# Optimization experiments

Measured on AMD Instinct MI355X. Metric: run time of the kernel, lower is better.

The kernel has to match this reference:

```python
import jax, jax.numpy as jnp
import numpy as np

B, T, F_IN = 4, 2048, 768
G, V = 2, 320          # num_groups, num_vars per group
VQ_DIM = 256
D = VQ_DIM // G        # var_dim = 128


def setup_inputs() -> dict:
    key = jax.random.key(0)
    k1, k2, k3 = jax.random.split(key, 3)
    x = jax.random.normal(k1, (B, T, F_IN), dtype=jnp.float32)
    # weight_proj: Linear(input_dim -> G*V), weight init N(0,1), bias zeros
    W = jax.random.normal(k2, (G * V, F_IN), dtype=jnp.float32)
    b = jnp.zeros((G * V,), dtype=jnp.float32)
    # self.vars: uniform_(0,1), stored here reshaped as [G, V, D]
    codebook = jax.random.uniform(k3, (G, V, D), dtype=jnp.float32)
    return {"x": x, "W": W, "b": b, "codebook": codebook}


def reference(x, W, b, codebook):
    bsz, tsz, fsz = x.shape
    g, v, d = codebook.shape
    # projection to logits over (group, codeword)
    logits = (x.reshape(-1, fsz) @ W.T + b).reshape(-1, g, v)  # [BT, G, V]
    k = jnp.argmax(logits, axis=-1)                            # [BT, G] int
    # hard one-hot stats (code perplexity)
    hard = jax.nn.one_hot(k, v, dtype=jnp.float32)             # [BT, G, V]
    hard_probs = hard.mean(axis=0)                             # [G, V]
    code_perplexity = jnp.exp(-jnp.sum(hard_probs * jnp.log(hard_probs + 1e-7), axis=-1)).sum()
    # soft stats (prob perplexity)
    avg_probs = jax.nn.softmax(logits.astype(jnp.float32), axis=-1).mean(axis=0)  # [G, V]
    prob_perplexity = jnp.exp(-jnp.sum(avg_probs * jnp.log(avg_probs + 1e-7), axis=-1)).sum()
    # eval path: hard one-hot times codebook summed == direct gather of codewords
    xq = codebook[jnp.arange(g)[None, :], k]                   # [BT, G, D]
    xq = xq.reshape(bsz, tsz, g * d)                           # [B, T, vq_dim]
    return xq, g * v, code_perplexity, prob_perplexity
```

## Files before the change

kernel.cpp:

```cpp
#include <hip/hip_runtime.h>
#include <hip/hip_bf16.h>

#define NROWS 8192
#define KDIM  768
#define VSZ   320
#define GSZ   2
#define NCOL  640
#define DSZ   128
#define BM    64
#define NMT   (NROWS / BM)
#define NBLK  (NMT * 2)
#define XQ_TOTAL (NROWS * GSZ * DSZ)
#define MARGIN 0.75f
#define NSHARD 8

typedef __attribute__((ext_vector_type(8))) short bf16x8;
typedef __attribute__((ext_vector_type(4))) float f32x4;

static __device__ __forceinline__ short f2bf(float f) {
    union { __hip_bfloat16 h; short s; } u;
    u.h = __float2bfloat16(f);
    return u.s;
}

static __device__ __forceinline__ void gload_lds16(const void* g, void* l) {
    __builtin_amdgcn_global_load_lds(
        (const __attribute__((address_space(1))) void*)g,
        (__attribute__((address_space(3))) void*)l, 16, 0, 0);
}

__global__ __launch_bounds__(256) void prep_w_k(const float* __restrict__ W,
                                                short* __restrict__ Wb,
                                                float* __restrict__ accf) {
    if (blockIdx.x < 20) {
        const int i = blockIdx.x * 256 + threadIdx.x;
        accf[i] = 0.f;
        accf[i + 5120] = 0.f;
    }
    const int id   = blockIdx.x * 256 + threadIdx.x;
    const int lane = id & 63;
    const int f    = id >> 6;
    const int n    = f % 5;
    const int t2   = f / 5;
    const int hc   = t2 & 7;
    const int kb   = t2 >> 3;
    const int col  = (hc * 5 + n) * 16 + (lane & 15);
    const int k    = kb * 32 + (lane >> 4) * 8;
    const float4 a = *(const float4*)(W + (size_t)col * KDIM + k);
    const float4 c = *(const float4*)(W + (size_t)col * KDIM + k + 4);
    bf16x8 r;
    r[0] = f2bf(a.x); r[1] = f2bf(a.y); r[2] = f2bf(a.z); r[3] = f2bf(a.w);
    r[4] = f2bf(c.x); r[5] = f2bf(c.y); r[6] = f2bf(c.z); r[7] = f2bf(c.w);
    *(bf16x8*)(Wb + (size_t)id * 8) = r;
}

#define STAGEB(kb64, BUF) do {                                                 \
    _Pragma("unroll")                                                          \
    for (int j = 0; j < 3; ++j) {                                              \
        const int rm = (j == 0) ? w : (j == 1) ? (w + 16) : (32 + (w & 7));    \
        const int kf = rm / 20, rr = rm % 20;                                  \
        const short* srcp = Wb + ((size_t)((2 * (kb64) + kf) * 8 + hc0 + rr / 5) * 5 + rr % 5) * 512; \
        gload_lds16(srcp + lane * 8, (char*)(BUF) + 8192 + rm * 1024);         \
    }                                                                          \
} while (0)

#define AWRITE(BUF, v) do {                                                    \
    const short s0 = f2bf((v).x), s1 = f2bf((v).y);                            \
    const short s2 = f2bf((v).z), s3 = f2bf((v).w);                            \
    const int lo = (s0 & 0xffff) | ((int)s1 << 16);                            \
    const int hi = (s2 & 0xffff) | ((int)s3 << 16);                            \
    *(int2*)((char*)(BUF) + a_off) = make_int2(lo, hi);                        \
} while (0)

#define COMPUTE(BUF) do {                                                      \
    const char* _bp = (const char*)(BUF);                                      \
    const bf16x8 a0 = *(const bf16x8*)(_bp + (rs * 2 + 0) * 1024 + lane * 16); \
    const bf16x8 a1 = *(const bf16x8*)(_bp + (rs * 2 + 1) * 1024 + lane * 16); \
    bf16x8 b0_[5], b1_[5];                                                     \
    _Pragma("unroll")                                                          \
    for (int n = 0; n < 5; ++n) {                                              \
        b0_[n] = *(const bf16x8*)(_bp + 8192 + (cc * 5 + n) * 1024 + lane * 16);      \
        b1_[n] = *(const bf16x8*)(_bp + 8192 + (20 + cc * 5 + n) * 1024 + lane * 16); \
    }                                                                          \
    _Pragma("unroll")                                                          \
    for (int n = 0; n < 5; ++n)                                                \
        acc[n] = __builtin_amdgcn_mfma_f32_16x16x32_bf16(a0, b0_[n], acc[n], 0, 0, 0); \
    _Pragma("unroll")                                                          \
    for (int n = 0; n < 5; ++n)                                                \
        acc[n] = __builtin_amdgcn_mfma_f32_16x16x32_bf16(a1, b1_[n], acc[n], 0, 0, 0); \
} while (0)

#define SYNC(N) do {                                                           \
    asm volatile("s_waitcnt vmcnt(" #N ") lgkmcnt(0)" ::: "memory");           \
    __builtin_amdgcn_sched_barrier(0);                                         \
    __builtin_amdgcn_s_barrier();                                              \
} while (0)

#define PH(kk, BA, BS, BC) do {                                                \
    AWRITE(BA, xv1);                                                           \
    xv1 = xv2;                                                                 \
    STAGEB((kk) + 2, BS);                                                      \
    xv2 = *(const float4*)(xrow + ((kk) + 3) * 64);                            \
    COMPUTE(BC);                                                               \
    SYNC(4);                                                                   \
} while (0)

__global__ __launch_bounds__(1024, 4) void fused_vq_k(
    const short* __restrict__ Wb,
    const float* __restrict__ x, const float* __restrict__ W,
    const float* __restrict__ b, const float* __restrict__ codebook,
    float* __restrict__ accf, float* __restrict__ xq) {

    __shared__ __align__(16) char bufs[3][48 * 1024];
    __shared__ float pacc[4][VSZ];
    __shared__ float cnt_f[VSZ];
    __shared__ float wmax[BM][4];
    __shared__ int   warg[BM][4];
    __shared__ float ssum[BM][4];
    __shared__ float rmax_s[BM];
    __shared__ int   rarg_s[BM];
    __shared__ int   cnt_s[BM];
    __shared__ int   list_s[BM][16];
    __shared__ int   code_s[BM];
    __shared__ int   work_s[BM];
    __shared__ int   nwork_s;

    const int tid   = threadIdx.x;
    const int lane  = tid & 63;
    const int w     = tid >> 6;
    const int l15   = lane & 15;
    const int l4    = lane >> 4;
    const int xcd   = (int)blockIdx.x & 7;
    const int sb    = xcd * (NBLK / 8) + ((int)blockIdx.x >> 3);
    const int mt    = sb >> 1;
    const int h     = sb & 1;
    const int row0  = mt * BM;
    const int rs    = w >> 2;
    const int cc    = w & 3;
    const int rbase = rs * 16;
    const int hc0   = h * 4;
    const int nf0   = h * 20 + cc * 5;

    float* accs = accf + (size_t)xcd * (2 * NCOL);

    const int arow  = tid >> 4;
    const int akk4  = (tid & 15) * 4;
    const int a_off = ((arow >> 4) * 2 + (akk4 >> 5)) * 1024 +
                      ((arow & 15) + 16 * ((akk4 >> 3) & 3)) * 16 + (akk4 & 4) * 2;
    const float* xrow = x + (size_t)(row0 + arow) * KDIM + akk4;

    for (int i = tid; i < VSZ; i += 1024) cnt_f[i] = 0.f;
    if (tid < BM) cnt_s[tid] = 0;
    if (tid == 0) nwork_s = 0;

    char* B0 = bufs[0];
    char* B1 = bufs[1];
    char* B2 = bufs[2];

    f32x4 acc[5];
#pragma unroll
    for (int n = 0; n < 5; ++n) acc[n] = (f32x4){0.f, 0.f, 0.f, 0.f};

    float4 xv1, xv2;
    {
        const float4 xq0 = *(const float4*)(xrow);
        STAGEB(0, B0);
        AWRITE(B0, xq0);
        xv1 = *(const float4*)(xrow + 64);
        STAGEB(1, B1);
        xv2 = *(const float4*)(xrow + 128);
        SYNC(4);
    }

#pragma unroll 1
    for (int t = 0; t < 3; ++t) {
        PH(3 * t + 0, B1, B2, B0);
        PH(3 * t + 1, B2, B0, B1);
        PH(3 * t + 2, B0, B1, B2);
    }
    AWRITE(B1, xv1);
    xv1 = xv2;
    STAGEB(11, B2);
    COMPUTE(B0);
    SYNC(4);
    AWRITE(B2, xv1);
    COMPUTE(B1);
    SYNC(0);
    COMPUTE(B2);

#pragma unroll
    for (int n = 0; n < 5; ++n) {
        const float bv = b[(nf0 + n) * 16 + l15];
#pragma unroll
        for (int r = 0; r < 4; ++r) acc[n][r] += bv;
    }

    float m4[4]; int a4[4];
#pragma unroll
    for (int r = 0; r < 4; ++r) { m4[r] = -3.4e38f; a4[r] = 0x7fffffff; }
#pragma unroll
    for (int n = 0; n < 5; ++n) {
        const int col = (nf0 + n) * 16 + l15;
#pragma unroll
        for (int r = 0; r < 4; ++r) {
            const float v = acc[n][r];
            if (v > m4[r]) { m4[r] = v; a4[r] = col; }
        }
    }
#pragma unroll
    for (int off = 8; off >= 1; off >>= 1)
#pragma unroll
        for (int r = 0; r < 4; ++r) {
            const float om = __shfl_xor(m4[r], off);
            const int   oa = __shfl_xor(a4[r], off);
            if (om > m4[r] || (om == m4[r] && oa < a4[r])) { m4[r] = om; a4[r] = oa; }
        }
    if (l15 == 0)
#pragma unroll
        for (int r = 0; r < 4; ++r) {
            const int row = rbase + l4 * 4 + r;
            wmax[row][cc] = m4[r];
            warg[row][cc] = a4[r];
        }
    __syncthreads();

    if (tid < BM) {
        float m = -3.4e38f; int c = 0x7fffffff;
#pragma unroll
        for (int q = 0; q < 4; ++q) {
            const float mq = wmax[tid][q];
            const int   cq = warg[tid][q];
            if (mq > m || (mq == m && cq < c)) { m = mq; c = cq; }
        }
        rmax_s[tid] = m;
        rarg_s[tid] = c;
    }
    __syncthreads();

    float rm[4];
#pragma unroll
    for (int r = 0; r < 4; ++r) rm[r] = rmax_s[rbase + l4 * 4 + r];
    float sden[4] = {0.f, 0.f, 0.f, 0.f};
#pragma unroll
    for (int n = 0; n < 5; ++n) {
        const int col = (nf0 + n) * 16 + l15;
#pragma unroll
        for (int r = 0; r < 4; ++r) {
            const float v = acc[n][r];
            if (v > rm[r] - MARGIN) {
                const int row = rbase + l4 * 4 + r;
                const int idx = atomicAdd(&cnt_s[row], 1);
                if (idx < 16) list_s[row][idx] = col;
            }
            const float e = __expf(v - rm[r]);
            acc[n][r] = e;
            sden[r] += e;
        }
    }
#pragma unroll
    for (int off = 8; off >= 1; off >>= 1)
#pragma unroll
        for (int r = 0; r < 4; ++r) sden[r] += __shfl_xor(sden[r], off);
    if (l15 == 0)
#pragma unroll
        for (int r = 0; r < 4; ++r) ssum[rbase + l4 * 4 + r][cc] = sden[r];
    __syncthreads();

    if (tid < BM) {
        if (cnt_s[tid] <= 1) {
            code_s[tid] = rarg_s[tid];
        } else {
            const int wi = atomicAdd(&nwork_s, 1);
            work_s[wi] = tid;
        }
    }

    float inv[4];
#pragma unroll
    for (int r = 0; r < 4; ++r) {
        const int row = rbase + l4 * 4 + r;
        inv[r] = 1.f / (ssum[row][0] + ssum[row][1] + ssum[row][2] + ssum[row][3]);
    }
#pragma unroll
    for (int n = 0; n < 5; ++n) {
        float pc = 0.f;
#pragma unroll
        for (int r = 0; r < 4; ++r) pc += acc[n][r] * inv[r];
        pc += __shfl_xor(pc, 16);
        pc += __shfl_xor(pc, 32);
        if (l4 == 0) pacc[rs][(nf0 + n) * 16 + l15 - h * VSZ] = pc;
    }
    __syncthreads();

    const int nwork = nwork_s;
    for (int it = w; it < nwork; it += 16) {
        const int row  = work_s[it];
        const int grow = row0 + row;
        const int nc   = min(cnt_s[row], 16);
        const float4* xr = (const float4*)(x + (size_t)grow * KDIM);
        float bestv = -3.4e38f; int bestc = 0x7fffffff;
        for (int ci = 0; ci < nc; ++ci) {
            const int col = list_s[row][ci];
            const float4* wr = (const float4*)(W + (size_t)col * KDIM);
            float p = 0.f;
#pragma unroll
            for (int j = 0; j < 3; ++j) {
                const float4 xa = xr[lane + 64 * j];
                const float4 wa = wr[lane + 64 * j];
                p += xa.x * wa.x + xa.y * wa.y + xa.z * wa.z + xa.w * wa.w;
            }
#pragma unroll
            for (int off = 32; off >= 1; off >>= 1) p += __shfl_xor(p, off);
            p += b[col];
            if (p > bestv || (p == bestv && col < bestc)) { bestv = p; bestc = col; }
        }
        if (lane == 0) code_s[row] = bestc;
    }
    __syncthreads();

    if (tid < BM) atomicAdd(&cnt_f[code_s[tid] - h * VSZ], 1.f);

#pragma unroll
    for (int u = 0; u < 2; ++u) {
        const int f   = tid + u * 1024;
        const int row = f >> 5;
        const int d4  = (f & 31) * 4;
        const int k   = code_s[row];
        const float4 v = *(const float4*)(codebook + (size_t)k * DSZ + d4);
        *(float4*)(xq + (size_t)(row0 + row) * (GSZ * DSZ) + h * DSZ + d4) = v;
    }
    __syncthreads();

    for (int i = tid; i < VSZ; i += 1024) {
        atomicAdd(&accs[h * VSZ + i], cnt_f[i]);
        atomicAdd(&accs[NCOL + h * VSZ + i],
                  pacc[0][i] + pacc[1][i] + pacc[2][i] + pacc[3][i]);
    }
}

__global__ __launch_bounds__(640) void finalize_k(const float* __restrict__ accf,
                                                  float* __restrict__ out_scalars) {
    __shared__ float se_c[GSZ], se_p[GSZ];
    const int t = threadIdx.x;
    if (t < GSZ) { se_c[t] = 0.f; se_p[t] = 0.f; }
    __syncthreads();
    const int g = t / VSZ;
    float sc = 0.f, sp = 0.f;
#pragma unroll
    for (int s = 0; s < NSHARD; ++s) {
        sc += accf[(size_t)s * (2 * NCOL) + t];
        sp += accf[(size_t)s * (2 * NCOL) + NCOL + t];
    }
    const float hp = sc * (1.f / (float)NROWS);
    const float ap = sp * (1.f / (float)NROWS);
    float tc = hp * logf(hp + 1e-7f);
    float tp = ap * logf(ap + 1e-7f);
#pragma unroll
    for (int off = 32; off >= 1; off >>= 1) {
        tc += __shfl_xor(tc, off);
        tp += __shfl_xor(tp, off);
    }
    if ((t & 63) == 0) { atomicAdd(&se_c[g], tc); atomicAdd(&se_p[g], tp); }
    __syncthreads();
    if (t == 0) {
        out_scalars[0] = (float)NCOL;
        out_scalars[1] = expf(-se_c[0]) + expf(-se_c[1]);
        out_scalars[2] = expf(-se_p[0]) + expf(-se_p[1]);
    }
}

extern "C" void kernel_launch(void* const* d_in, const int* in_sizes, int n_in,
                              void* d_out, int out_size, void* d_ws, size_t ws_size,
                              hipStream_t stream) {
    const float* x        = (const float*)d_in[0];
    const float* W        = (const float*)d_in[1];
    const float* b        = (const float*)d_in[2];
    const float* codebook = (const float*)d_in[3];
    float* out = (float*)d_out;

    short* Wb   = (short*)d_ws;
    float* accf = (float*)((char*)d_ws + 983040);

    prep_w_k<<<dim3(240), dim3(256), 0, stream>>>(W, Wb, accf);
    fused_vq_k<<<dim3(NBLK), dim3(1024), 0, stream>>>(Wb, x, W, b, codebook,
                                                      accf, out);
    finalize_k<<<dim3(1), dim3(640), 0, stream>>>(accf, out + XQ_TOTAL);
}
```

Measured before the change: 37.17 us.

## Transpose logits through LDS for per-wave row epilogue with ballot-based candidate rescoring

After the GEMM, the logits are written to shared memory with a padded stride. Each wave then handles four whole rows: argmax and softmax use wave-wide shuffles, and near-max candidates are found with ballots instead of shared-memory atomic lists. This removes several block-wide barriers and the cross-wave reduction arrays, and the fp32 rescoring of ambiguous rows is spread across every wave. The cost is an extra LDS write and read of the logits, plus per-wave divergence when a row needs rescoring.

```diff
diff --git a/kernel.cpp b/kernel.cpp
--- a/kernel.cpp
+++ b/kernel.cpp
@@ -13,6 +13,7 @@
 #define XQ_TOTAL (NROWS * GSZ * DSZ)
 #define MARGIN 0.75f
 #define NSHARD 8
+#define LSTRIDE 322
 
 typedef __attribute__((ext_vector_type(8))) short bf16x8;
 typedef __attribute__((ext_vector_type(4))) float f32x4;
@@ -112,18 +113,8 @@
     float* __restrict__ accf, float* __restrict__ xq) {
 
     __shared__ __align__(16) char bufs[3][48 * 1024];
-    __shared__ float pacc[4][VSZ];
+    __shared__ float pacc1[VSZ];
     __shared__ float cnt_f[VSZ];
-    __shared__ float wmax[BM][4];
-    __shared__ int   warg[BM][4];
-    __shared__ float ssum[BM][4];
-    __shared__ float rmax_s[BM];
-    __shared__ int   rarg_s[BM];
-    __shared__ int   cnt_s[BM];
-    __shared__ int   list_s[BM][16];
-    __shared__ int   code_s[BM];
-    __shared__ int   work_s[BM];
-    __shared__ int   nwork_s;
 
     const int tid   = threadIdx.x;
     const int lane  = tid & 63;
@@ -149,9 +140,7 @@
                       ((arow & 15) + 16 * ((akk4 >> 3) & 3)) * 16 + (akk4 & 4) * 2;
     const float* xrow = x + (size_t)(row0 + arow) * KDIM + akk4;
 
-    for (int i = tid; i < VSZ; i += 1024) cnt_f[i] = 0.f;
-    if (tid < BM) cnt_s[tid] = 0;
-    if (tid == 0) nwork_s = 0;
+    for (int i = tid; i < VSZ; i += 1024) { cnt_f[i] = 0.f; pacc1[i] = 0.f; }
 
     char* B0 = bufs[0];
     char* B1 = bufs[1];
@@ -188,144 +177,93 @@
     SYNC(0);
     COMPUTE(B2);
 
+    float* lgs = (float*)bufs;
 #pragma unroll
     for (int n = 0; n < 5; ++n) {
         const float bv = b[(nf0 + n) * 16 + l15];
-#pragma unroll
-        for (int r = 0; r < 4; ++r) acc[n][r] += bv;
-    }
-
-    float m4[4]; int a4[4];
-#pragma unroll
-    for (int r = 0; r < 4; ++r) { m4[r] = -3.4e38f; a4[r] = 0x7fffffff; }
-#pragma unroll
-    for (int n = 0; n < 5; ++n) {
-        const int col = (nf0 + n) * 16 + l15;
-#pragma unroll
-        for (int r = 0; r < 4; ++r) {
-            const float v = acc[n][r];
-            if (v > m4[r]) { m4[r] = v; a4[r] = col; }
+        const int cl = (cc * 5 + n) * 16 + l15;
+#pragma unroll
+        for (int r = 0; r < 4; ++r)
+            lgs[(rbase + l4 * 4 + r) * LSTRIDE + cl] = acc[n][r] + bv;
+    }
+    __syncthreads();
+
+    float preg[5] = {0.f, 0.f, 0.f, 0.f, 0.f};
+    int codes[4];
+#pragma unroll
+    for (int r = 0; r < 4; ++r) {
+        const int row = 4 * w + r;
+        float l[5];
+#pragma unroll
+        for (int q = 0; q < 5; ++q) l[q] = lgs[row * LSTRIDE + lane + 64 * q];
+        float m = l[0]; int amq = 0;
+#pragma unroll
+        for (int q = 1; q < 5; ++q) if (l[q] > m) { m = l[q]; amq = q; }
+        int acol = lane + 64 * amq;
+#pragma unroll
+        for (int off = 32; off >= 1; off >>= 1) {
+            const float om = __shfl_xor(m, off);
+            const int   oc = __shfl_xor(acol, off);
+            if (om > m || (om == m && oc < acol)) { m = om; acol = oc; }
         }
-    }
-#pragma unroll
-    for (int off = 8; off >= 1; off >>= 1)
-#pragma unroll
-        for (int r = 0; r < 4; ++r) {
-            const float om = __shfl_xor(m4[r], off);
-            const int   oa = __shfl_xor(a4[r], off);
-            if (om > m4[r] || (om == m4[r] && oa < a4[r])) { m4[r] = om; a4[r] = oa; }
+        unsigned long long mask[5];
+        int total = 0;
+#pragma unroll
+        for (int q = 0; q < 5; ++q) {
+            mask[q] = __ballot(l[q] > m - MARGIN);
+            total += __popcll(mask[q]);
         }
-    if (l15 == 0)
-#pragma unroll
-        for (int r = 0; r < 4; ++r) {
-            const int row = rbase + l4 * 4 + r;
-            wmax[row][cc] = m4[r];
-            warg[row][cc] = a4[r];
+        float s = 0.f;
+#pragma unroll
+        for (int q = 0; q < 5; ++q) { l[q] = __expf(l[q] - m); s += l[q]; }
+#pragma unroll
+        for (int off = 32; off >= 1; off >>= 1) s += __shfl_xor(s, off);
+        const float inv = 1.f / s;
+#pragma unroll
+        for (int q = 0; q < 5; ++q) preg[q] += l[q] * inv;
+
+        int code = acol;
+        if (total > 1) {
+            const int grow = row0 + row;
+            const float4* xr = (const float4*)(x + (size_t)grow * KDIM);
+            float bestv = -3.4e38f; int bestc = 0x7fffffff;
+#pragma unroll 1
+            for (int q = 0; q < 5; ++q) {
+                unsigned long long mm = mask[q];
+                while (mm) {
+                    const int bit = __ffsll((long long)mm) - 1;
+                    mm &= mm - 1;
+                    const int cl = bit + 64 * q;
+                    const int colg = h * VSZ + cl;
+                    const float4* wr = (const float4*)(W + (size_t)colg * KDIM);
+                    float p = 0.f;
+#pragma unroll
+                    for (int j = 0; j < 3; ++j) {
+                        const float4 xa = xr[lane + 64 * j];
+                        const float4 wa = wr[lane + 64 * j];
+                        p += xa.x * wa.x + xa.y * wa.y + xa.z * wa.z + xa.w * wa.w;
+                    }
+#pragma unroll
+                    for (int off = 32; off >= 1; off >>= 1) p += __shfl_xor(p, off);
+                    p += b[colg];
+                    if (p > bestv || (p == bestv && cl < bestc)) { bestv = p; bestc = cl; }
+                }
+            }
+            code = bestc;
         }
-    __syncthreads();
-
-    if (tid < BM) {
-        float m = -3.4e38f; int c = 0x7fffffff;
-#pragma unroll
-        for (int q = 0; q < 4; ++q) {
-            const float mq = wmax[tid][q];
-            const int   cq = warg[tid][q];
-            if (mq > m || (mq == m && cq < c)) { m = mq; c = cq; }
-        }
-        rmax_s[tid] = m;
-        rarg_s[tid] = c;
-    }
-    __syncthreads();
-
-    float rm[4];
-#pragma unroll
-    for (int r = 0; r < 4; ++r) rm[r] = rmax_s[rbase + l4 * 4 + r];
-    float sden[4] = {0.f, 0.f, 0.f, 0.f};
-#pragma unroll
-    for (int n = 0; n < 5; ++n) {
-        const int col = (nf0 + n) * 16 + l15;
-#pragma unroll
-        for (int r = 0; r < 4; ++r) {
-            const float v = acc[n][r];
-            if (v > rm[r] - MARGIN) {
-                const int row = rbase + l4 * 4 + r;
-                const int idx = atomicAdd(&cnt_s[row], 1);
-                if (idx < 16) list_s[row][idx] = col;
-            }
-            const float e = __expf(v - rm[r]);
-            acc[n][r] = e;
-            sden[r] += e;
-        }
-    }
-#pragma unroll
-    for (int off = 8; off >= 1; off >>= 1)
-#pragma unroll
-        for (int r = 0; r < 4; ++r) sden[r] += __shfl_xor(sden[r], off);
-    if (l15 == 0)
-#pragma unroll
-        for (int r = 0; r < 4; ++r) ssum[rbase + l4 * 4 + r][cc] = sden[r];
-    __syncthreads();
-
-    if (tid < BM) {
-        if (cnt_s[tid] <= 1) {
-            code_s[tid] = rarg_s[tid];
-        } else {
-            const int wi = atomicAdd(&nwork_s, 1);
-            work_s[wi] = tid;
-        }
-    }
-
-    float inv[4];
-#pragma unroll
-    for (int r = 0; r < 4; ++r) {
-        const int row = rbase + l4 * 4 + r;
-        inv[r] = 1.f / (ssum[row][0] + ssum[row][1] + ssum[row][2] + ssum[row][3]);
-    }
-#pragma unroll
-    for (int n = 0; n < 5; ++n) {
-        float pc = 0.f;
-#pragma unroll
-        for (int r = 0; r < 4; ++r) pc += acc[n][r] * inv[r];
-        pc += __shfl_xor(pc, 16);
-        pc += __shfl_xor(pc, 32);
-        if (l4 == 0) pacc[rs][(nf0 + n) * 16 + l15 - h * VSZ] = pc;
-    }
-    __syncthreads();
-
-    const int nwork = nwork_s;
-    for (int it = w; it < nwork; it += 16) {
-        const int row  = work_s[it];
-        const int grow = row0 + row;
-        const int nc   = min(cnt_s[row], 16);
-        const float4* xr = (const float4*)(x + (size_t)grow * KDIM);
-        float bestv = -3.4e38f; int bestc = 0x7fffffff;
-        for (int ci = 0; ci < nc; ++ci) {
-            const int col = list_s[row][ci];
-            const float4* wr = (const float4*)(W + (size_t)col * KDIM);
-            float p = 0.f;
-#pragma unroll
-            for (int j = 0; j < 3; ++j) {
-                const float4 xa = xr[lane + 64 * j];
-                const float4 wa = wr[lane + 64 * j];
-                p += xa.x * wa.x + xa.y * wa.y + xa.z * wa.z + xa.w * wa.w;
-            }
-#pragma unroll
-            for (int off = 32; off >= 1; off >>= 1) p += __shfl_xor(p, off);
-            p += b[col];
-            if (p > bestv || (p == bestv && col < bestc)) { bestv = p; bestc = col; }
-        }
-        if (lane == 0) code_s[row] = bestc;
-    }
-    __syncthreads();
-
-    if (tid < BM) atomicAdd(&cnt_f[code_s[tid] - h * VSZ], 1.f);
+        codes[r] = __shfl(code, 0);
+        if (lane == 0) atomicAdd(&cnt_f[codes[r]], 1.f);
+    }
+
+#pragma unroll
+    for (int q = 0; q < 5; ++q) atomicAdd(&pacc1[lane + 64 * q], preg[q]);
 
 #pragma unroll
     for (int u = 0; u < 2; ++u) {
-        const int f   = tid + u * 1024;
-        const int row = f >> 5;
-        const int d4  = (f & 31) * 4;
-        const int k   = code_s[row];
+        const int rr  = 2 * u + (lane >> 5);
+        const int row = 4 * w + rr;
+        const int d4  = (lane & 31) * 4;
+        const int k   = h * VSZ + codes[rr];
         const float4 v = *(const float4*)(codebook + (size_t)k * DSZ + d4);
         *(float4*)(xq + (size_t)(row0 + row) * (GSZ * DSZ) + h * DSZ + d4) = v;
     }
@@ -333,8 +271,7 @@
 
     for (int i = tid; i < VSZ; i += 1024) {
         atomicAdd(&accs[h * VSZ + i], cnt_f[i]);
-        atomicAdd(&accs[NCOL + h * VSZ + i],
-                  pacc[0][i] + pacc[1][i] + pacc[2][i] + pacc[3][i]);
+        atomicAdd(&accs[NCOL + h * VSZ + i], pacc1[i]);
     }
 }
 
```

Measured after the change: 42.96 us. 1.16x slower.
